# Kernel optimization log

Measured on AMD Instinct MI355X. Metric: run time of the kernel, lower is better.

## Reference

```python
import jax, jax.numpy as jnp
import numpy as np

N_HEAD = 16
N_KV = 4
HEAD_DIM = 128
EPS = float(np.finfo(np.float32).eps)  # torch F.rms_norm default eps


def _rope_tables(T, half, dtype=jnp.float32):
    inv_freq = 1.0 / (10000.0 ** (jnp.arange(half, dtype=dtype) / half))
    ang = jnp.arange(T, dtype=dtype)[:, None] * inv_freq[None, :]  # (T, half)
    cos = jnp.cos(ang)[None, :, None, :]  # (1, T, 1, half)
    sin = jnp.sin(ang)[None, :, None, :]
    return cos, sin


def setup_inputs() -> dict:
    key = jax.random.key(0)
    ks = jax.random.split(key, 5)
    B, T, C = 2, 2048, 2048
    x = jax.random.normal(ks[0], (B, T, C), dtype=jnp.float32)
    cos, sin = _rope_tables(T, HEAD_DIM // 2)
    s = 0.02
    W_Q = jax.random.normal(ks[1], (C, N_HEAD * HEAD_DIM), dtype=jnp.float32) * s
    W_K = jax.random.normal(ks[2], (C, N_KV * HEAD_DIM), dtype=jnp.float32) * s
    W_V = jax.random.normal(ks[3], (C, N_KV * HEAD_DIM), dtype=jnp.float32) * s
    W_O = jax.random.normal(ks[4], (C, C), dtype=jnp.float32) * s
    return {"x": x, "cos": cos, "sin": sin, "W_Q": W_Q, "W_K": W_K, "W_V": W_V, "W_O": W_O}


def _apply_rope(x, cos, sin):
    # x: (B,T,H,D); cos/sin: (1,T,1,D/2)
    d = x.shape[-1] // 2
    x1, x2 = x[..., :d], x[..., d:]
    return jnp.concatenate([x1 * cos + x2 * sin, -x1 * sin + x2 * cos], axis=-1)


def _rms_norm(x):
    return x * jax.lax.rsqrt(jnp.mean(x * x, axis=-1, keepdims=True) + EPS)


def reference(x, cos, sin, W_Q, W_K, W_V, W_O):
    B, T, C = x.shape
    G = N_HEAD // N_KV  # kv groups
    q = (x @ W_Q).reshape(B, T, N_HEAD, HEAD_DIM)
    k = (x @ W_K).reshape(B, T, N_KV, HEAD_DIM)
    v = (x @ W_V).reshape(B, T, N_KV, HEAD_DIM)
    q = _rms_norm(_apply_rope(q, cos[:, :T], sin[:, :T]))
    k = _rms_norm(_apply_rope(k, cos[:, :T], sin[:, :T]))
    # GQA: avoid materializing expanded K/V; group q by kv head
    qg = q.reshape(B, T, N_KV, G, HEAD_DIM)
    scale = 1.0 / jnp.sqrt(jnp.asarray(HEAD_DIM, dtype=x.dtype))
    scores = jnp.einsum("btkgd,bskd->bkgts", qg, k) * scale  # (B,Kv,G,T,T)
    causal = jnp.tril(jnp.ones((T, T), dtype=bool))
    scores = jnp.where(causal, scores, jnp.asarray(-jnp.inf, dtype=scores.dtype))
    attn = jax.nn.softmax(scores, axis=-1)
    out = jnp.einsum("bkgts,bskd->btkgd", attn, v).reshape(B, T, C)
    return out @ W_O
```

## Files before the change

kernel.cpp:

```cpp
#include <hip/hip_runtime.h>
#include <hip/hip_bf16.h>
#include <stdint.h>

typedef __bf16 bf16_4 __attribute__((ext_vector_type(4)));
typedef __bf16 bf16_8 __attribute__((ext_vector_type(8)));
typedef float f32x4 __attribute__((ext_vector_type(4)));

#define AS1 __attribute__((address_space(1)))
#define AS3 __attribute__((address_space(3)))

__device__ __forceinline__ void gload_lds16(const void* g, void* l) {
  __builtin_amdgcn_global_load_lds((const AS1 void*)g, (AS3 void*)l, 16, 0, 0);
}

__global__ void detect_dtype(const void* __restrict__ cosT, int* __restrict__ flag) {
  uint32_t w = *reinterpret_cast<const uint32_t*>(cosT);
  *flag = ((w & 0xFFFFu) == 0x3F80u) ? 1 : 0;
}

__global__ __launch_bounds__(256) void prep_all(const void* __restrict__ cosT,
                                                const void* __restrict__ sinT,
                                                const void* __restrict__ x,
                                                const void* __restrict__ WQ,
                                                const void* __restrict__ WK,
                                                const void* __restrict__ WV,
                                                const void* __restrict__ WO,
                                                float* __restrict__ csF,
                                                __bf16* __restrict__ xb,
                                                __bf16* __restrict__ Wt,
                                                __bf16* __restrict__ WOt,
                                                const int* __restrict__ flag) {
  const int blk = blockIdx.x, tid = threadIdx.x;
  const bool isb = (*flag != 0);
  if (blk < 512) {
    const int i = blk * 256 + tid;
    if (isb) {
      csF[i]          = (float)reinterpret_cast<const __bf16*>(cosT)[i];
      csF[131072 + i] = (float)reinterpret_cast<const __bf16*>(sinT)[i];
    } else {
      csF[i]          = reinterpret_cast<const float*>(cosT)[i];
      csF[131072 + i] = reinterpret_cast<const float*>(sinT)[i];
    }
    return;
  }
  if (blk < 4608) {
    const int i = (blk - 512) * 256 + tid;
    if (isb) {
      reinterpret_cast<int4*>(xb)[i] = reinterpret_cast<const int4*>(x)[i];
    } else {
      const float4* s = reinterpret_cast<const float4*>(x);
      const float4 a = s[2 * i], c = s[2 * i + 1];
      __bf16 o[8] = {(__bf16)a.x, (__bf16)a.y, (__bf16)a.z, (__bf16)a.w,
                     (__bf16)c.x, (__bf16)c.y, (__bf16)c.z, (__bf16)c.w};
      reinterpret_cast<int4*>(xb)[i] = *reinterpret_cast<int4*>(o);
    }
    return;
  }
  __shared__ __bf16 t[32][33];
  const int tb = blk - 4608;
  const int bx = tb % 160, by = tb / 160;
  const int tx = tid & 31, ty = tid >> 5;
  const void* src;
  __bf16* dst;
  int C, c0;
  if (bx < 64)      { src = WQ; dst = Wt;                        C = 2048; c0 = bx * 32; }
  else if (bx < 80) { src = WK; dst = Wt + (size_t)2048 * 2048;  C = 512;  c0 = (bx - 64) * 32; }
  else if (bx < 96) { src = WV; dst = Wt + (size_t)2560 * 2048;  C = 512;  c0 = (bx - 80) * 32; }
  else              { src = WO; dst = WOt;                       C = 2048; c0 = (bx - 96) * 32; }
  const int r0 = by * 32;
  #pragma unroll
  for (int i = 0; i < 32; i += 8) {
    const size_t idx = (size_t)(r0 + ty + i) * C + c0 + tx;
    t[ty + i][tx] = isb ? reinterpret_cast<const __bf16*>(src)[idx]
                        : (__bf16)reinterpret_cast<const float*>(src)[idx];
  }
  __syncthreads();
  #pragma unroll
  for (int i = 0; i < 32; i += 8)
    dst[(size_t)(c0 + ty + i) * 2048 + r0 + tx] = t[tx][ty + i];
}

template <int DYN>
__global__ __launch_bounds__(512) void gemm8p(const __bf16* __restrict__ A,
                                              const __bf16* __restrict__ Bt,
                                              void* __restrict__ Cv,
                                              int M, int N, int K,
                                              const int* __restrict__ flag) {
  __shared__ __attribute__((aligned(16))) __bf16 As[2][128 * 64];
  __shared__ __attribute__((aligned(16))) __bf16 Bs[2][256 * 64];
  const int tid = threadIdx.x;
  const int lane = tid & 63, w = tid >> 6;
  const int wm = w >> 2, wn = w & 3;
  const int r = lane & 15, g = lane >> 4;
  const int q8 = gridDim.x >> 3;
  const int wg = (blockIdx.x & 7) * q8 + (blockIdx.x >> 3);
  const int gx = M >> 7;
  const int bm = (wg % gx) * 128, bn = (wg / gx) * 256;
  const bool isb = DYN ? (*flag != 0) : true;
  const int NT = K >> 6;

  f32x4 acc[4][4] = {};

#define STA(kt, p, j)                                                              \
  {                                                                                \
    const int o_ = tid * 16 + (j) * 8192;                                          \
    const int row_ = o_ >> 7, blk_ = (o_ >> 4) & 7;                                \
    gload_lds16(A + (size_t)(bm + row_) * K + (kt) * 64 + ((blk_ ^ (row_ & 7)) << 3), \
                (char*)As[p] + o_);                                                \
  }
#define STB(kt, p, j)                                                              \
  {                                                                                \
    const int o_ = tid * 16 + (j) * 8192;                                          \
    const int rl_ = o_ >> 7, blk_ = (o_ >> 4) & 7;                                 \
    const int gr_ = ((rl_ >> 5) & 3) * 64 + ((rl_ >> 7) & 1) * 32 + (rl_ & 31);    \
    gload_lds16(Bt + (size_t)(bn + gr_) * K + (kt) * 64 + ((blk_ ^ (rl_ & 7)) << 3), \
                (char*)Bs[p] + o_);                                                \
  }

  STA(0, 0, 0); STA(0, 0, 1);
  STB(0, 0, 0); STB(0, 0, 1); STB(0, 0, 2); STB(0, 0, 3);
  asm volatile("s_waitcnt vmcnt(2)\ns_barrier" ::: "memory");

  for (int kt = 0; kt < NT; ++kt) {
    const int cur = kt & 1, nxt = cur ^ 1;
    const bool pf = (kt + 1 < NT);
    const char* Ac = (const char*)As[cur];
    const char* Bc = (const char*)Bs[cur];

    bf16_8 af[4][2], bf[2][2];
    #pragma unroll
    for (int m = 0; m < 4; ++m)
      #pragma unroll
      for (int kk = 0; kk < 2; ++kk) {
        const int row = wm * 64 + m * 16 + r;
        af[m][kk] = *reinterpret_cast<const bf16_8*>(
            Ac + row * 128 + (((kk * 4 + g) ^ (row & 7)) << 4));
      }
    #pragma unroll
    for (int n = 0; n < 2; ++n)
      #pragma unroll
      for (int kk = 0; kk < 2; ++kk) {
        const int rl = wn * 32 + n * 16 + r;
        bf[n][kk] = *reinterpret_cast<const bf16_8*>(
            Bc + rl * 128 + (((kk * 4 + g) ^ (rl & 7)) << 4));
      }
    if (pf) { STA(kt + 1, nxt, 0); STA(kt + 1, nxt, 1); STB(kt + 1, nxt, 0); }
    __builtin_amdgcn_s_barrier();
    __builtin_amdgcn_s_setprio(1);
    #pragma unroll
    for (int kk = 0; kk < 2; ++kk)
      #pragma unroll
      for (int m = 0; m < 4; ++m)
        #pragma unroll
        for (int n = 0; n < 2; ++n)
          acc[m][n] = __builtin_amdgcn_mfma_f32_16x16x32_bf16(af[m][kk], bf[n][kk], acc[m][n], 0, 0, 0);
    __builtin_amdgcn_s_setprio(0);
    if (pf) asm volatile("s_waitcnt vmcnt(3)\ns_barrier" ::: "memory");
    else    asm volatile("s_waitcnt vmcnt(0)\ns_barrier" ::: "memory");

    bf16_8 bg[2][2];
    #pragma unroll
    for (int n = 0; n < 2; ++n)
      #pragma unroll
      for (int kk = 0; kk < 2; ++kk) {
        const int rl = 128 + wn * 32 + n * 16 + r;
        bg[n][kk] = *reinterpret_cast<const bf16_8*>(
            Bc + rl * 128 + (((kk * 4 + g) ^ (rl & 7)) << 4));
      }
    if (pf) { STB(kt + 1, nxt, 1); STB(kt + 1, nxt, 2); STB(kt + 1, nxt, 3); }
    __builtin_amdgcn_s_barrier();
    __builtin_amdgcn_s_setprio(1);
    #pragma unroll
    for (int kk = 0; kk < 2; ++kk)
      #pragma unroll
      for (int m = 0; m < 4; ++m)
        #pragma unroll
        for (int n = 0; n < 2; ++n)
          acc[m][n + 2] = __builtin_amdgcn_mfma_f32_16x16x32_bf16(af[m][kk], bg[n][kk], acc[m][n + 2], 0, 0, 0);
    __builtin_amdgcn_s_setprio(0);
    if (pf) asm volatile("s_waitcnt vmcnt(2)\ns_barrier" ::: "memory");
    else    asm volatile("s_waitcnt vmcnt(0)\ns_barrier" ::: "memory");
  }
#undef STA
#undef STB

  #pragma unroll
  for (int m = 0; m < 4; ++m)
    #pragma unroll
    for (int n = 0; n < 4; ++n)
      #pragma unroll
      for (int j = 0; j < 4; ++j) {
        const int row = bm + wm * 64 + m * 16 + g * 4 + j;
        const int col = bn + wn * 64 + n * 16 + r;
        const float v = acc[m][n][j];
        if (isb) reinterpret_cast<__bf16*>(Cv)[(size_t)row * N + col] = (__bf16)v;
        else     reinterpret_cast<float*>(Cv)[(size_t)row * N + col] = v;
      }
}

__global__ __launch_bounds__(256) void rope_vtrans(__bf16* __restrict__ qkv,
                                                   const float* __restrict__ csF,
                                                   __bf16* __restrict__ vt) {
  const int blk = blockIdx.x, tid = threadIdx.x;
  if (blk < 20480) {
    const int gw = blk * 4 + (tid >> 6);
    const int lane = tid & 63;
    const int head = gw % 20;
    const int m = gw / 20;
    const int t = m & 2047;
    __bf16* p = qkv + (size_t)m * 3072 + head * 128;
    const float x1 = (float)p[lane];
    const float x2 = (float)p[lane + 64];
    const float c = csF[t * 64 + lane];
    const float s = csF[131072 + t * 64 + lane];
    const float y1 = x1 * c + x2 * s;
    const float y2 = x2 * c - x1 * s;
    float ss = y1 * y1 + y2 * y2;
    #pragma unroll
    for (int mk = 32; mk >= 1; mk >>= 1) ss += __shfl_xor(ss, mk, 64);
    float inv = rsqrtf(ss * (1.0f / 128.0f) + 1.1920929e-7f);
    if (head < 16) inv *= 0.12751743f;
    p[lane] = (__bf16)(y1 * inv);
    p[lane + 64] = (__bf16)(y2 * inv);
    return;
  }
  __shared__ __bf16 t[32][33];
  const int vb = blk - 20480;
  const int z = vb >> 10, rem = vb & 1023;
  const int x = rem & 63, y = rem >> 6;
  const int tx = tid & 31, ty = tid >> 5;
  const int t0 = x * 32, c0 = y * 32;
  #pragma unroll
  for (int i = 0; i < 32; i += 8)
    t[ty + i][tx] = qkv[(size_t)(z * 2048 + t0 + ty + i) * 3072 + 2560 + c0 + tx];
  __syncthreads();
  #pragma unroll
  for (int i = 0; i < 32; i += 8)
    vt[(size_t)(z * 512 + c0 + ty + i) * 2048 + t0 + tx] = t[tx][ty + i];
}

__global__ __launch_bounds__(256) void attn_fwd7(const __bf16* __restrict__ qkv,
                                                 const __bf16* __restrict__ vt,
                                                 __bf16* __restrict__ out) {
  __shared__ __attribute__((aligned(16))) __bf16 Kl[64 * 128];
  __shared__ __attribute__((aligned(16))) __bf16 Vl[128 * 64];
  __shared__ __attribute__((aligned(16))) __bf16 Pl[4][16][64];

  const int tid = threadIdx.x, lane = tid & 63, w = tid >> 6;
  const int r = lane & 15, g = lane >> 4;
  const int lid = blockIdx.x;
  const int grp = lid & 7, inner = lid >> 3;
  const int b = grp >> 2, kvh = grp & 3;
  const int h = kvh * 4 + (inner & 3);
  const int qt = 31 - (inner >> 2);
  const int nt = qt + 1;
  const __bf16* Kbase = qkv + (size_t)(b * 2048) * 3072 + 2048 + kvh * 128;
  const __bf16* Vbase = vt + (size_t)((b * 4 + kvh) * 128) * 2048;

#define STAGE(kt)                                                               \
  {                                                                             \
    _Pragma("unroll")                                                           \
    for (int i_ = 0; i_ < 4; ++i_) {                                            \
      const int o_ = tid * 16 + i_ * 4096;                                      \
      const int krow_ = o_ >> 8;                                                \
      const int jj_ = (o_ >> 4) & 15;                                           \
      const int gj_ = (jj_ & 8) | ((jj_ ^ krow_) & 7);                          \
      gload_lds16(Kbase + (size_t)((kt) * 64 + krow_) * 3072 + gj_ * 8,         \
                  (char*)Kl + o_);                                              \
      const int d_ = o_ >> 7;                                                   \
      const int j2_ = (o_ >> 4) & 7;                                            \
      const int g2_ = j2_ ^ (d_ & 7);                                           \
      gload_lds16(Vbase + (size_t)d_ * 2048 + (kt) * 64 + g2_ * 8,              \
                  (char*)Vl + o_);                                              \
    }                                                                           \
  }

  bf16_8 qf[4];
  {
    const __bf16* qp = qkv + (size_t)(b * 2048 + qt * 64 + w * 16 + r) * 3072 + h * 128 + g * 8;
    #pragma unroll
    for (int kb = 0; kb < 4; ++kb) qf[kb] = *reinterpret_cast<const bf16_8*>(qp + kb * 32);
  }

  char* const plw = (char*)Pl + w * 2048;
  f32x4 accO[8] = {};
  float mst = -1e30f, lst = 0.0f;

  for (int kt = 0; kt < nt; ++kt) {
    STAGE(kt);
    asm volatile("s_waitcnt vmcnt(0)" ::: "memory");
    __syncthreads();

    f32x4 sacc[4] = {};
    #pragma unroll
    for (int kb = 0; kb < 4; ++kb) {
      const int jj = kb * 4 + g;
      const int jp = (jj & 8) | ((jj ^ (r & 7)) & 7);
      #pragma unroll
      for (int n = 0; n < 4; ++n) {
        const bf16_8 kf = *reinterpret_cast<const bf16_8*>((char*)Kl + (n * 16 + r) * 256 + jp * 16);
        sacc[n] = __builtin_amdgcn_mfma_f32_16x16x32_bf16(kf, qf[kb], sacc[n], 0, 0, 0);
      }
    }

    float p[4][4];
    float pm = -1e30f;
    #pragma unroll
    for (int n = 0; n < 4; ++n)
      #pragma unroll
      for (int j = 0; j < 4; ++j) {
        p[n][j] = sacc[n][j];
        pm = fmaxf(pm, p[n][j]);
      }
    if (kt == qt) {
      const int qpos = qt * 64 + w * 16 + r;
      pm = -1e30f;
      #pragma unroll
      for (int n = 0; n < 4; ++n)
        #pragma unroll
        for (int j = 0; j < 4; ++j) {
          if (kt * 64 + n * 16 + g * 4 + j > qpos) p[n][j] = -1e30f;
          pm = fmaxf(pm, p[n][j]);
        }
    }
    pm = fmaxf(pm, __shfl_xor(pm, 16, 64));
    pm = fmaxf(pm, __shfl_xor(pm, 32, 64));

    float mn = mst;
    if (!__all(pm - mst <= 12.0f)) {
      mn = fmaxf(mst, pm);
      const float alpha = exp2f(mst - mn);
      mst = mn;
      lst *= alpha;
      float av[4];
      #pragma unroll
      for (int j = 0; j < 4; ++j) av[j] = __shfl(alpha, g * 4 + j, 64);
      #pragma unroll
      for (int dt = 0; dt < 8; ++dt)
        #pragma unroll
        for (int j = 0; j < 4; ++j) accO[dt][j] *= av[j];
    }
    float rs = 0.0f;
    #pragma unroll
    for (int n = 0; n < 4; ++n)
      #pragma unroll
      for (int j = 0; j < 4; ++j) {
        p[n][j] = exp2f(p[n][j] - mn);
        rs += p[n][j];
      }
    rs += __shfl_xor(rs, 16, 64);
    rs += __shfl_xor(rs, 32, 64);
    lst += rs;

    #pragma unroll
    for (int n = 0; n < 4; ++n) {
      bf16_4 pk;
      #pragma unroll
      for (int j = 0; j < 4; ++j) pk[j] = (__bf16)p[n][j];
      const int blk = 2 * n + (g >> 1);
      char* pw = plw + r * 128 + ((blk ^ (r & 7)) << 4) + (g & 1) * 8;
      *reinterpret_cast<bf16_4*>(pw) = pk;
    }

    #pragma unroll
    for (int half = 0; half < 2; ++half) {
      const bf16_8 pa = *reinterpret_cast<const bf16_8*>(
          plw + r * 128 + (((half * 4 + g) ^ (r & 7)) << 4));
      #pragma unroll
      for (int dt = 0; dt < 8; ++dt) {
        const int d = dt * 16 + r;
        const bf16_8 vf = *reinterpret_cast<const bf16_8*>((char*)Vl + d * 128 + ((half * 4 + g) ^ (d & 7)) * 16);
        accO[dt] = __builtin_amdgcn_mfma_f32_16x16x32_bf16(pa, vf, accO[dt], 0, 0, 0);
      }
    }

    __syncthreads();
  }

  float lv[4];
  #pragma unroll
  for (int j = 0; j < 4; ++j) lv[j] = 1.0f / __shfl(lst, g * 4 + j, 64);
  #pragma unroll
  for (int dt = 0; dt < 8; ++dt)
    #pragma unroll
    for (int j = 0; j < 4; ++j) {
      const int t = qt * 64 + w * 16 + g * 4 + j;
      out[(size_t)(b * 2048 + t) * 2048 + h * 128 + dt * 16 + r] = (__bf16)(accO[dt][j] * lv[j]);
    }
#undef STAGE
}

extern "C" void kernel_launch(void* const* d_in, const int* in_sizes, int n_in,
                              void* d_out, int out_size, void* d_ws, size_t ws_size,
                              hipStream_t stream) {
  const void* x    = d_in[0];
  const void* cosT = d_in[1];
  const void* sinT = d_in[2];
  const void* W_Q  = d_in[3];
  const void* W_K  = d_in[4];
  const void* W_V  = d_in[5];
  const void* W_O  = d_in[6];

  const int B = 2, T = 2048, C = 2048;
  const int M = B * T;
  const int NQKV = 3072;

  char* ws = (char*)d_ws;
  int*    flag = (int*)ws;                       ws += 256;
  float*  csF  = (float*)ws;                     ws += (size_t)2 * 131072 * 4;
  __bf16* xb   = (__bf16*)ws;                    ws += (size_t)M * C * 2;
  __bf16* Wt   = (__bf16*)ws;                    ws += (size_t)NQKV * C * 2;
  __bf16* WOt  = (__bf16*)ws;                    ws += (size_t)C * C * 2;
  __bf16* QKV  = (__bf16*)ws;                    ws += (size_t)M * NQKV * 2;
  __bf16* AO   = (__bf16*)ws;                    ws += (size_t)M * C * 2;
  __bf16* VT   = xb;

  detect_dtype<<<1, 1, 0, stream>>>(cosT, flag);
  prep_all<<<dim3(14848), 256, 0, stream>>>(cosT, sinT, x, W_Q, W_K, W_V, W_O,
                                            csF, xb, Wt, WOt, flag);
  gemm8p<0><<<dim3((M / 128) * (NQKV / 256)), 512, 0, stream>>>(xb, Wt, QKV, M, NQKV, C, flag);
  rope_vtrans<<<dim3(22528), 256, 0, stream>>>(QKV, csF, VT);
  attn_fwd7<<<dim3(1024), 256, 0, stream>>>(QKV, VT, AO);
  gemm8p<1><<<dim3((M / 128) * (C / 256)), 512, 0, stream>>>(AO, WOt, d_out, M, C, C, flag);
}
```

Before: 229.2 us.

## Double-buffer attention K/V tiles with 32-key blocks and prefetch

Attention now works on 32-key tiles instead of 64 and double-buffers K and V in shared memory, issuing async global-to-LDS loads for the next tile before computing the current one. This overlaps memory loads with MFMA and softmax work, replacing the old serial load-wait-compute loop. LDS use stays about the same. The cost is twice as many iterations, each with its own barriers, row-max and sum reductions, and possible rescaling. The swizzle patterns are adjusted to the narrower tiles.

```diff
diff --git a/kernel.cpp b/kernel.cpp
--- a/kernel.cpp
+++ b/kernel.cpp
@@ -239,12 +239,12 @@
     vt[(size_t)(z * 512 + c0 + ty + i) * 2048 + t0 + tx] = t[tx][ty + i];
 }
 
-__global__ __launch_bounds__(256) void attn_fwd7(const __bf16* __restrict__ qkv,
+__global__ __launch_bounds__(256) void attn_fwd9(const __bf16* __restrict__ qkv,
                                                  const __bf16* __restrict__ vt,
                                                  __bf16* __restrict__ out) {
-  __shared__ __attribute__((aligned(16))) __bf16 Kl[64 * 128];
-  __shared__ __attribute__((aligned(16))) __bf16 Vl[128 * 64];
-  __shared__ __attribute__((aligned(16))) __bf16 Pl[4][16][64];
+  __shared__ __attribute__((aligned(16))) __bf16 Kl[2][32 * 128];
+  __shared__ __attribute__((aligned(16))) __bf16 Vl[2][128 * 32];
+  __shared__ __attribute__((aligned(16))) __bf16 Pl[4 * 16 * 32];
 
   const int tid = threadIdx.x, lane = tid & 63, w = tid >> 6;
   const int r = lane & 15, g = lane >> 4;
@@ -253,25 +253,26 @@
   const int b = grp >> 2, kvh = grp & 3;
   const int h = kvh * 4 + (inner & 3);
   const int qt = 31 - (inner >> 2);
-  const int nt = qt + 1;
+  const int nt = 2 * (qt + 1);
   const __bf16* Kbase = qkv + (size_t)(b * 2048) * 3072 + 2048 + kvh * 128;
   const __bf16* Vbase = vt + (size_t)((b * 4 + kvh) * 128) * 2048;
-
-#define STAGE(kt)                                                               \
+  const int kr = (r & 3) ^ ((r >> 2) & 3);
+
+#define STAGE(kt, p)                                                            \
   {                                                                             \
     _Pragma("unroll")                                                           \
-    for (int i_ = 0; i_ < 4; ++i_) {                                            \
+    for (int i_ = 0; i_ < 2; ++i_) {                                            \
       const int o_ = tid * 16 + i_ * 4096;                                      \
-      const int krow_ = o_ >> 8;                                                \
+      const int krow_ = o_ >> 8;                                     \
       const int jj_ = (o_ >> 4) & 15;                                           \
       const int gj_ = (jj_ & 8) | ((jj_ ^ krow_) & 7);                          \
-      gload_lds16(Kbase + (size_t)((kt) * 64 + krow_) * 3072 + gj_ * 8,         \
-                  (char*)Kl + o_);                                              \
-      const int d_ = o_ >> 7;                                                   \
-      const int j2_ = (o_ >> 4) & 7;                                            \
-      const int g2_ = j2_ ^ (d_ & 7);                                           \
-      gload_lds16(Vbase + (size_t)d_ * 2048 + (kt) * 64 + g2_ * 8,              \
-                  (char*)Vl + o_);                                              \
+      gload_lds16(Kbase + (size_t)((kt) * 32 + krow_) * 3072 + gj_ * 8,         \
+                  (char*)Kl[p] + o_);                                           \
+      const int d_ = o_ >> 6;                                       \
+      const int j2_ = (o_ >> 4) & 3;                                            \
+      const int g2_ = j2_ ^ (d_ & 3) ^ ((d_ >> 2) & 3);                         \
+      gload_lds16(Vbase + (size_t)d_ * 2048 + (kt) * 32 + g2_ * 8,              \
+                  (char*)Vl[p] + o_);                                           \
     }                                                                           \
   }
 
@@ -282,44 +283,51 @@
     for (int kb = 0; kb < 4; ++kb) qf[kb] = *reinterpret_cast<const bf16_8*>(qp + kb * 32);
   }
 
-  char* const plw = (char*)Pl + w * 2048;
+  char* const plw = (char*)Pl + w * 1024;
   f32x4 accO[8] = {};
   float mst = -1e30f, lst = 0.0f;
 
+  STAGE(0, 0);
   for (int kt = 0; kt < nt; ++kt) {
-    STAGE(kt);
-    asm volatile("s_waitcnt vmcnt(0)" ::: "memory");
+    const int cur = kt & 1;
+    const bool pf = (kt + 1 < nt);
+    if (pf) STAGE(kt + 1, cur ^ 1);
+    if (pf) asm volatile("s_waitcnt vmcnt(4)" ::: "memory");
+    else    asm volatile("s_waitcnt vmcnt(0)" ::: "memory");
     __syncthreads();
 
-    f32x4 sacc[4] = {};
+    const char* Kc = (const char*)Kl[cur];
+    const char* Vc = (const char*)Vl[cur];
+
+    f32x4 sacc[2] = {};
     #pragma unroll
     for (int kb = 0; kb < 4; ++kb) {
       const int jj = kb * 4 + g;
       const int jp = (jj & 8) | ((jj ^ (r & 7)) & 7);
       #pragma unroll
-      for (int n = 0; n < 4; ++n) {
-        const bf16_8 kf = *reinterpret_cast<const bf16_8*>((char*)Kl + (n * 16 + r) * 256 + jp * 16);
+      for (int n = 0; n < 2; ++n) {
+        const bf16_8 kf = *reinterpret_cast<const bf16_8*>(Kc + (n * 16 + r) * 256 + jp * 16);
         sacc[n] = __builtin_amdgcn_mfma_f32_16x16x32_bf16(kf, qf[kb], sacc[n], 0, 0, 0);
       }
     }
 
-    float p[4][4];
+    float p[2][4];
     float pm = -1e30f;
     #pragma unroll
-    for (int n = 0; n < 4; ++n)
+    for (int n = 0; n < 2; ++n)
       #pragma unroll
       for (int j = 0; j < 4; ++j) {
         p[n][j] = sacc[n][j];
         pm = fmaxf(pm, p[n][j]);
       }
-    if (kt == qt) {
+    if (kt >= 2 * qt) {
       const int qpos = qt * 64 + w * 16 + r;
       pm = -1e30f;
       #pragma unroll
-      for (int n = 0; n < 4; ++n)
+      for (int n = 0; n < 2; ++n)
         #pragma unroll
         for (int j = 0; j < 4; ++j) {
-          if (kt * 64 + n * 16 + g * 4 + j > qpos) p[n][j] = -1e30f;
+          if (kt * 32 + n * 16 + g * 4 + j > qpos) p[n][j] = -1e30f;
           pm = fmaxf(pm, p[n][j]);
         }
     }
@@ -342,7 +350,7 @@
     }
     float rs = 0.0f;
     #pragma unroll
-    for (int n = 0; n < 4; ++n)
+    for (int n = 0; n < 2; ++n)
       #pragma unroll
       for (int j = 0; j < 4; ++j) {
         p[n][j] = exp2f(p[n][j] - mn);
@@ -353,25 +361,22 @@
     lst += rs;
 
     #pragma unroll
-    for (int n = 0; n < 4; ++n) {
+    for (int n = 0; n < 2; ++n) {
       bf16_4 pk;
       #pragma unroll
       for (int j = 0; j < 4; ++j) pk[j] = (__bf16)p[n][j];
       const int blk = 2 * n + (g >> 1);
-      char* pw = plw + r * 128 + ((blk ^ (r & 7)) << 4) + (g & 1) * 8;
+      char* pw = plw + r * 64 + ((blk ^ kr) << 4) + (g & 1) * 8;
       *reinterpret_cast<bf16_4*>(pw) = pk;
     }
 
-    #pragma unroll
-    for (int half = 0; half < 2; ++half) {
-      const bf16_8 pa = *reinterpret_cast<const bf16_8*>(
-          plw + r * 128 + (((half * 4 + g) ^ (r & 7)) << 4));
-      #pragma unroll
-      for (int dt = 0; dt < 8; ++dt) {
-        const int d = dt * 16 + r;
-        const bf16_8 vf = *reinterpret_cast<const bf16_8*>((char*)Vl + d * 128 + ((half * 4 + g) ^ (d & 7)) * 16);
-        accO[dt] = __builtin_amdgcn_mfma_f32_16x16x32_bf16(pa, vf, accO[dt], 0, 0, 0);
-      }
+    const bf16_8 pa = *reinterpret_cast<const bf16_8*>(plw + r * 64 + ((g ^ kr) << 4));
+    #pragma unroll
+    for (int dt = 0; dt < 8; ++dt) {
+      const int d = dt * 16 + r;
+      const int kd = (d & 3) ^ ((d >> 2) & 3);
+      const bf16_8 vf = *reinterpret_cast<const bf16_8*>(Vc + d * 64 + ((g ^ kd) << 4));
+      accO[dt] = __builtin_amdgcn_mfma_f32_16x16x32_bf16(pa, vf, accO[dt], 0, 0, 0);
     }
 
     __syncthreads();
@@ -420,6 +425,6 @@
                                             csF, xb, Wt, WOt, flag);
   gemm8p<0><<<dim3((M / 128) * (NQKV / 256)), 512, 0, stream>>>(xb, Wt, QKV, M, NQKV, C, flag);
   rope_vtrans<<<dim3(22528), 256, 0, stream>>>(QKV, csF, VT);
-  attn_fwd7<<<dim3(1024), 256, 0, stream>>>(QKV, VT, AO);
+  attn_fwd9<<<dim3(1024), 256, 0, stream>>>(QKV, VT, AO);
   gemm8p<1><<<dim3((M / 128) * (C / 256)), 512, 0, stream>>>(AO, WOt, d_out, M, C, C, flag);
 }
```

Measured after the change: 245.2 us. +7.0%, slower.

## Use 128x384 tile GEMM for QKV projection with staged B-tile pipelining

Applied to the files above, without the earlier changes.

Adds a new GEMM kernel with a 128x384 output tile for the QKV projection, so the grid becomes 32x8 = 256 workgroups, one per CU on the MI355X. The kernel splits each K step into three sub-phases over the B tile and interleaves the next-tile prefetch loads with the MFMA work using explicit vmcnt waits and barriers. It aims to remove the partial second wave of the old 32x12 grid and to raise reuse of the A tile. In exchange it uses more LDS and more accumulator registers, which can lower occupancy, and the hand-counted waitcnt values must match the number of outstanding loads.

```diff
diff --git a/kernel.cpp b/kernel.cpp
--- a/kernel.cpp
+++ b/kernel.cpp
@@ -198,6 +198,155 @@
       }
 }
 
+template <int DYN>
+__global__ __launch_bounds__(512) void gemm8p3(const __bf16* __restrict__ A,
+                                               const __bf16* __restrict__ Bt,
+                                               void* __restrict__ Cv,
+                                               int M, int N, int K,
+                                               const int* __restrict__ flag) {
+  __shared__ __attribute__((aligned(16))) __bf16 As[2][128 * 64];
+  __shared__ __attribute__((aligned(16))) __bf16 Bs[2][384 * 64];
+  const int tid = threadIdx.x;
+  const int lane = tid & 63, w = tid >> 6;
+  const int wm = w >> 2, wn = w & 3;
+  const int r = lane & 15, g = lane >> 4;
+  const int q8 = gridDim.x >> 3;
+  const int wg = (blockIdx.x & 7) * q8 + (blockIdx.x >> 3);
+  const int gx = M >> 7;
+  const int bm = (wg % gx) * 128, bn = (wg / gx) * 384;
+  const bool isb = DYN ? (*flag != 0) : true;
+  const int NT = K >> 6;
+
+  f32x4 acc[4][6] = {};
+
+#define STA3(kt, p, j)                                                             \
+  {                                                                                \
+    const int o_ = tid * 16 + (j) * 8192;                                          \
+    const int row_ = o_ >> 7, blk_ = (o_ >> 4) & 7;                                \
+    gload_lds16(A + (size_t)(bm + row_) * K + (kt) * 64 + ((blk_ ^ (row_ & 7)) << 3), \
+                (char*)As[p] + o_);                                                \
+  }
+#define STB3(kt, p, j)                                                             \
+  {                                                                                \
+    const int o_ = tid * 16 + (j) * 8192;                                          \
+    const int rl_ = o_ >> 7, blk_ = (o_ >> 4) & 7;                                 \
+    const int gr_ = ((rl_ & 127) >> 5) * 96 + (rl_ >> 7) * 32 + (rl_ & 31);        \
+    gload_lds16(Bt + (size_t)(bn + gr_) * K + (kt) * 64 + ((blk_ ^ (rl_ & 7)) << 3), \
+                (char*)Bs[p] + o_);                                                \
+  }
+
+  STA3(0, 0, 0); STA3(0, 0, 1);
+  STB3(0, 0, 0); STB3(0, 0, 1); STB3(0, 0, 2);
+  STB3(0, 0, 3); STB3(0, 0, 4); STB3(0, 0, 5);
+  asm volatile("s_waitcnt vmcnt(4)\ns_barrier" ::: "memory");
+
+  for (int kt = 0; kt < NT; ++kt) {
+    const int cur = kt & 1, nxt = cur ^ 1;
+    const bool pf = (kt + 1 < NT);
+    const char* Ac = (const char*)As[cur];
+    const char* Bc = (const char*)Bs[cur];
+    bf16_8 af[4][2];
+
+    {
+      #pragma unroll
+      for (int m = 0; m < 4; ++m)
+        #pragma unroll
+        for (int kk = 0; kk < 2; ++kk) {
+          const int row = wm * 64 + m * 16 + r;
+          af[m][kk] = *reinterpret_cast<const bf16_8*>(
+              Ac + row * 128 + (((kk * 4 + g) ^ (row & 7)) << 4));
+        }
+      bf16_8 bf[2][2];
+      #pragma unroll
+      for (int n = 0; n < 2; ++n)
+        #pragma unroll
+        for (int kk = 0; kk < 2; ++kk) {
+          const int rl = wn * 32 + n * 16 + r;
+          bf[n][kk] = *reinterpret_cast<const bf16_8*>(
+              Bc + rl * 128 + (((kk * 4 + g) ^ (r & 7)) << 4));
+        }
+      if (pf) { STA3(kt + 1, nxt, 0); STA3(kt + 1, nxt, 1); STB3(kt + 1, nxt, 0); }
+      __builtin_amdgcn_s_barrier();
+      __builtin_amdgcn_s_setprio(1);
+      #pragma unroll
+      for (int kk = 0; kk < 2; ++kk)
+        #pragma unroll
+        for (int m = 0; m < 4; ++m)
+          #pragma unroll
+          for (int n = 0; n < 2; ++n)
+            acc[m][n] = __builtin_amdgcn_mfma_f32_16x16x32_bf16(af[m][kk], bf[n][kk], acc[m][n], 0, 0, 0);
+      __builtin_amdgcn_s_setprio(0);
+      if (pf) asm volatile("s_waitcnt vmcnt(5)\ns_barrier" ::: "memory");
+      else    asm volatile("s_waitcnt vmcnt(0)\ns_barrier" ::: "memory");
+    }
+
+    {
+      bf16_8 bf[2][2];
+      #pragma unroll
+      for (int n = 0; n < 2; ++n)
+        #pragma unroll
+        for (int kk = 0; kk < 2; ++kk) {
+          const int rl = 128 + wn * 32 + n * 16 + r;
+          bf[n][kk] = *reinterpret_cast<const bf16_8*>(
+              Bc + rl * 128 + (((kk * 4 + g) ^ (r & 7)) << 4));
+        }
+      if (pf) { STB3(kt + 1, nxt, 1); STB3(kt + 1, nxt, 2); }
+      __builtin_amdgcn_s_barrier();
+      __builtin_amdgcn_s_setprio(1);
+      #pragma unroll
+      for (int kk = 0; kk < 2; ++kk)
+        #pragma unroll
+        for (int m = 0; m < 4; ++m)
+          #pragma unroll
+          for (int n = 0; n < 2; ++n)
+            acc[m][n + 2] = __builtin_amdgcn_mfma_f32_16x16x32_bf16(af[m][kk], bf[n][kk], acc[m][n + 2], 0, 0, 0);
+      __builtin_amdgcn_s_setprio(0);
+      if (pf) asm volatile("s_waitcnt vmcnt(5)\ns_barrier" ::: "memory");
+      else    asm volatile("s_waitcnt vmcnt(0)\ns_barrier" ::: "memory");
+    }
+
+    {
+      bf16_8 bf[2][2];
+      #pragma unroll
+      for (int n = 0; n < 2; ++n)
+        #pragma unroll
+        for (int kk = 0; kk < 2; ++kk) {
+          const int rl = 256 + wn * 32 + n * 16 + r;
+          bf[n][kk] = *reinterpret_cast<const bf16_8*>(
+              Bc + rl * 128 + (((kk * 4 + g) ^ (r & 7)) << 4));
+        }
+      if (pf) { STB3(kt + 1, nxt, 3); STB3(kt + 1, nxt, 4); STB3(kt + 1, nxt, 5); }
+      __builtin_amdgcn_s_barrier();
+      __builtin_amdgcn_s_setprio(1);
+      #pragma unroll
+      for (int kk = 0; kk < 2; ++kk)
+        #pragma unroll
+        for (int m = 0; m < 4; ++m)
+          #pragma unroll
+          for (int n = 0; n < 2; ++n)
+            acc[m][n + 4] = __builtin_amdgcn_mfma_f32_16x16x32_bf16(af[m][kk], bf[n][kk], acc[m][n + 4], 0, 0, 0);
+      __builtin_amdgcn_s_setprio(0);
+      if (pf) asm volatile("s_waitcnt vmcnt(4)\ns_barrier" ::: "memory");
+      else    asm volatile("s_waitcnt vmcnt(0)\ns_barrier" ::: "memory");
+    }
+  }
+#undef STA3
+#undef STB3
+
+  #pragma unroll
+  for (int m = 0; m < 4; ++m)
+    #pragma unroll
+    for (int n = 0; n < 6; ++n)
+      #pragma unroll
+      for (int j = 0; j < 4; ++j) {
+        const int row = bm + wm * 64 + m * 16 + g * 4 + j;
+        const int col = bn + wn * 96 + n * 16 + r;
+        const float v = acc[m][n][j];
+        if (isb) reinterpret_cast<__bf16*>(Cv)[(size_t)row * N + col] = (__bf16)v;
+        else     reinterpret_cast<float*>(Cv)[(size_t)row * N + col] = v;
+      }
+}
+
 __global__ __launch_bounds__(256) void rope_vtrans(__bf16* __restrict__ qkv,
                                                    const float* __restrict__ csF,
                                                    __bf16* __restrict__ vt) {
@@ -418,7 +567,7 @@
   detect_dtype<<<1, 1, 0, stream>>>(cosT, flag);
   prep_all<<<dim3(14848), 256, 0, stream>>>(cosT, sinT, x, W_Q, W_K, W_V, W_O,
                                             csF, xb, Wt, WOt, flag);
-  gemm8p<0><<<dim3((M / 128) * (NQKV / 256)), 512, 0, stream>>>(xb, Wt, QKV, M, NQKV, C, flag);
+  gemm8p3<0><<<dim3((M / 128) * (NQKV / 384)), 512, 0, stream>>>(xb, Wt, QKV, M, NQKV, C, flag);
   rope_vtrans<<<dim3(22528), 256, 0, stream>>>(QKV, csF, VT);
   attn_fwd7<<<dim3(1024), 256, 0, stream>>>(QKV, VT, AO);
   gemm8p<1><<<dim3((M / 128) * (C / 256)), 512, 0, stream>>>(AO, WOt, d_out, M, C, C, flag);
```

New measurement: 206.5 us. -9.9%, faster.
